# Performance work log

Measured on AMD Instinct MI355X. Metric: run time of the kernel, lower is better.

## Reference

```python
import jax, jax.numpy as jnp
import numpy as np

LEAK = 0.01  # torch LeakyReLU default negative_slope

def lrelu(x):
    return jnp.where(x >= 0, x, LEAK * x)

def edge_conv(x, src, dst, ea, W1, b1, W2, b2):
    # message: cat(x_i=target, x_j=source, edge_attr) -> Linear -> LeakyReLU -> Linear
    m = jnp.concatenate([x[dst], x[src], ea], axis=1)          # [E, 2F+Fe]
    h = lrelu(m @ W1 + b1) @ W2 + b2                            # [E, H]
    n = x.shape[0]
    agg = jnp.full((n, h.shape[1]), jnp.inf, h.dtype).at[dst].min(h)  # scatter-min at target
    return jnp.where(jnp.isfinite(agg), agg, jnp.zeros_like(agg))     # empty nodes -> 0


def setup_inputs() -> dict:
    key = jax.random.key(0)
    ks = jax.random.split(key, 20)
    B, N, E = 4, 20000, 640000
    NF, AD, EF, H = 2, 1, 1, 8
    inp = {
        "node_features": jax.random.randint(ks[0], (B, N, NF), 0, 10, dtype=jnp.int32),
        "actions": jax.random.normal(ks[1], (B, N), dtype=jnp.float32),
        "edge_index": jax.random.randint(ks[2], (B, 2, E), 0, N, dtype=jnp.int64),
        "edge_features": jax.random.normal(ks[3], (B, E, EF), dtype=jnp.float32),
    }
    d0 = NF + AD  # 3
    def lin(k, fin, fout):
        s = 1.0 / np.sqrt(fin)
        k1, k2 = jax.random.split(k)
        return (jax.random.uniform(k1, (fin, fout), jnp.float32, -s, s),
                jax.random.uniform(k2, (fout,), jnp.float32, -s, s))
    inp["c1_W1"], inp["c1_b1"] = lin(ks[4], 2 * d0 + EF, H)
    inp["c1_W2"], inp["c1_b2"] = lin(ks[5], H, H)
    inp["c2_W1"], inp["c2_b1"] = lin(ks[6], 2 * H + 1, H)
    inp["c2_W2"], inp["c2_b2"] = lin(ks[7], H, H)
    inp["c3_W1"], inp["c3_b1"] = lin(ks[8], 2 * H + 1, H)
    inp["c3_W2"], inp["c3_b2"] = lin(ks[9], H, H)
    inp["lin_W"], inp["lin_b"] = lin(ks[10], d0 + H, 1)
    return inp


def reference(node_features, actions, edge_index, edge_features,
              c1_W1, c1_b1, c1_W2, c1_b2,
              c2_W1, c2_b1, c2_W2, c2_b2,
              c3_W1, c3_b1, c3_W2, c3_b2,
              lin_W, lin_b):
    # x = int(node_features) concat actions  -> float
    x0 = jnp.concatenate([node_features.astype(jnp.int32).astype(jnp.float32),
                          actions[..., None]], axis=-1)  # [B,N,3]

    def per_graph(x0g, eig, eag):
        src, dst = eig[0], eig[1]  # flow source_to_target: x_j=src, x_i=dst
        h = lrelu(edge_conv(x0g, src, dst, eag, c1_W1, c1_b1, c1_W2, c1_b2))
        h = lrelu(edge_conv(h, src, dst, eag, c2_W1, c2_b1, c2_W2, c2_b2))
        h = lrelu(edge_conv(h, src, dst, eag, c3_W1, c3_b1, c3_W2, c3_b2))
        xc = jnp.concatenate([x0g, h], axis=1)  # [N, 3+8]
        return jnp.sum(xc, axis=0)              # sum-pool over nodes

    pooled = jax.vmap(per_graph)(x0, edge_index, edge_features)  # [B, 11]
    return pooled @ lin_W + lin_b  # [B, 1]
```

## Files before the change

kernel.cpp:

```cpp
#include <hip/hip_runtime.h>
#include <hip/hip_cooperative_groups.h>

namespace cg = cooperative_groups;

#define LEAK 0.01f
#define BS 128
#define PCHUNK 4096
#define PT 512
#define CT 512
#define MAXNB 256
#define CPGMAX 256

__device__ __forceinline__ float lrelu(float v) {
    return v >= 0.f ? v : LEAK * v;
}

__device__ __forceinline__ unsigned int fmin_encode(float x) {
    unsigned int u = __float_as_uint(x);
    return (u & 0x80000000u) ? ~u : (u | 0x80000000u);
}
__device__ __forceinline__ float fmin_decode(unsigned int k) {
    unsigned int u = (k & 0x80000000u) ? (k ^ 0x80000000u) : ~k;
    return __uint_as_float(u);
}

__device__ __forceinline__ unsigned int bf16_rne(float f) {
    unsigned int u = __float_as_uint(f);
    return (u + 0x7FFFu + ((u >> 16) & 1u)) >> 16;
}

__device__ __forceinline__ void block_add(float c, float* dst) {
    __shared__ float wsum[8];
#pragma unroll
    for (int off = 32; off > 0; off >>= 1) c += __shfl_down(c, off, 64);
    int lane = threadIdx.x & 63;
    int wave = threadIdx.x >> 6;
    if (lane == 0) wsum[wave] = c;
    __syncthreads();
    if (threadIdx.x == 0) {
        float s = 0.f;
        int nw = blockDim.x >> 6;
        for (int w = 0; w < nw; ++w) s += wsum[w];
        atomicAdd(dst, s);
    }
}


__device__ void init_slice_body(
    const int* __restrict__ nf, const float* __restrict__ act,
    const float* __restrict__ W1, const float* __restrict__ b1,
    const float* __restrict__ lw, const float* __restrict__ lb,
    float* __restrict__ a1, unsigned short* __restrict__ a2,
    float* __restrict__ out, int N, int b, int n0, int n1) {
    int t = threadIdx.x;
    float c = 0.f;
    for (int n = n0 + t; n < n1; n += PT) {
        size_t i = (size_t)b * N + n;
        float x0 = (float)nf[i * 2 + 0];
        float x1 = (float)nf[i * 2 + 1];
        float x2 = act[i];
        float v1[8], v2[8];
#pragma unroll
        for (int j = 0; j < 8; ++j) {
            v1[j] = b1[j] + x0 * W1[0 * 8 + j] + x1 * W1[1 * 8 + j] + x2 * W1[2 * 8 + j];
            v2[j] =         x0 * W1[3 * 8 + j] + x1 * W1[4 * 8 + j] + x2 * W1[5 * 8 + j];
        }
        float4* o1 = (float4*)(a1 + i * 8);
        o1[0] = make_float4(v1[0], v1[1], v1[2], v1[3]);
        o1[1] = make_float4(v1[4], v1[5], v1[6], v1[7]);
        unsigned int w[4];
#pragma unroll
        for (int q = 0; q < 4; ++q)
            w[q] = bf16_rne(v2[2 * q]) | (bf16_rne(v2[2 * q + 1]) << 16);
        *(int4*)(a2 + i * 8) = make_int4(w[0], w[1], w[2], w[3]);
        c += x0 * lw[0] + x1 * lw[1] + x2 * lw[2];
        if (n == 0) c += lb[0];
    }
    block_add(c, &out[b]);
}

__device__ void part_body(
    const int* __restrict__ ei, const float* __restrict__ ea,
    int2* __restrict__ pairs, int* __restrict__ ofs,
    int E, int NB, int CPG, int b, int c,
    int* __restrict__ lc, int* __restrict__ lofs, int* __restrict__ ts) {
    int t = threadIdx.x;
    for (int i = t; i < NB; i += PT) lc[i] = 0;
    __syncthreads();

    int e0 = c * PCHUNK;
    int end = min(e0 + PCHUNK, E);
    const int* srow = ei + (size_t)b * 2 * E;
    const int* drow = srow + E;

    int pk[PCHUNK / PT];
#pragma unroll
    for (int j = 0; j < PCHUNK / PT; ++j) {
        int e = e0 + j * PT + t;
        int p = -1;
        if (e < end) {
            int d = drow[e];
            int bin = d >> 7;
            int r = atomicAdd(&lc[bin], 1);
            p = bin | ((d & 127) << 10) | (r << 17);
        }
        pk[j] = p;
    }
    __syncthreads();

    int v = (t < NB) ? lc[t] : 0;
    ts[t] = v;
    __syncthreads();
    int incl = v;
    for (int off = 1; off < PT; off <<= 1) {
        int add = (t >= off) ? ts[t - off] : 0;
        __syncthreads();
        incl += add;
        ts[t] = incl;
        __syncthreads();
    }
    if (t < NB) lofs[t] = incl - v;
    if (t == PT - 1) lofs[NB] = incl;
    __syncthreads();

    for (int i = t; i <= NB; i += PT) {
        int w = lofs[i];
        ofs[((size_t)b * (NB + 1) + i) * CPG + c] = w;
        if (i < NB) lc[i] = w;
    }
    __syncthreads();

    size_t pbase = (size_t)b * E + e0;
#pragma unroll
    for (int j = 0; j < PCHUNK / PT; ++j) {
        int e = e0 + j * PT + t;
        if (e < end) {
            int p = pk[j];
            int bin = p & 1023;
            int dl = (p >> 10) & 127;
            int r = p >> 17;
            int pos = lc[bin] + r;
            pairs[pbase + pos] =
                make_int2(srow[e] | (dl << 16), __float_as_int(ea[(size_t)b * E + e]));
        }
    }
}

__device__ __forceinline__ void conv_edge_compute(
    const float* we, const float* bb, const float* __restrict__ W2,
    int2 p, int4 raw, const float* __restrict__ a1s,
    unsigned int* __restrict__ acc) {
    int dl = (p.x >> 16) & 127;
    float eav = __int_as_float(p.y);
    unsigned int wq[4] = {(unsigned int)raw.x, (unsigned int)raw.y,
                          (unsigned int)raw.z, (unsigned int)raw.w};
    float a2v[8];
#pragma unroll
    for (int q = 0; q < 4; ++q) {
        a2v[2 * q]     = __uint_as_float(wq[q] << 16);
        a2v[2 * q + 1] = __uint_as_float(wq[q] & 0xFFFF0000u);
    }
    float h1[8];
#pragma unroll
    for (int j = 0; j < 8; ++j) {
        h1[j] = a1s[dl * 9 + j] + a2v[j];
        h1[j] = fmaf(eav, we[j], h1[j]);
        h1[j] = lrelu(h1[j]);
    }
    float h2[8];
#pragma unroll
    for (int j = 0; j < 8; ++j) h2[j] = bb[j];
#pragma unroll
    for (int kk = 0; kk < 8; ++kk) {
        float hk = h1[kk];
#pragma unroll
        for (int j = 0; j < 8; ++j) h2[j] = fmaf(hk, W2[kk * 8 + j], h2[j]);
    }
#pragma unroll
    for (int j = 0; j < 8; ++j)
        atomicMin(&acc[dl * 9 + j], fmin_encode(h2[j]));
}

__device__ void conv_edges_runs(
    const unsigned short* __restrict__ a2g, const float* we, const float* bb,
    const float* __restrict__ W2, const int2* __restrict__ pairsg,
    const int* __restrict__ ofb, int CPG,
    const float* __restrict__ a1s, unsigned int* __restrict__ acc,
    int* __restrict__ rs, int* __restrict__ re) {
    int t = threadIdx.x;
    for (int c = t; c < CPG; c += CT) {
        rs[c] = ofb[c];
        re[c] = ofb[CPG + c];
    }
    __syncthreads();
    int sw = t >> 5, sub = t & 31;
    const int nsw = CT >> 5;
    for (int c = sw; c < CPG; c += nsw) {
        int cb = c * PCHUNK;
        int k1 = cb + re[c];
        for (int k = cb + rs[c] + sub; k < k1; k += 32) {
            int2 p = pairsg[k];
            int4 v = *(const int4*)(a2g + (size_t)(p.x & 0xFFFF) * 8);
            conv_edge_compute(we, bb, W2, p, v, a1s, acc);
        }
    }
}

__device__ void conv_mid_body(
    const float* __restrict__ a1, const unsigned short* __restrict__ a2,
    const float* __restrict__ w1e, const float* __restrict__ W2,
    const float* __restrict__ b2,
    const float* __restrict__ nW1, const float* __restrict__ nb1,
    const int* __restrict__ ofs, const int2* __restrict__ pairs,
    float* __restrict__ na1, unsigned short* __restrict__ na2,
    int N, int NB, int CPG, int E, int b, int bin,
    float* __restrict__ a1s, unsigned int* __restrict__ acc,
    int* __restrict__ rs, int* __restrict__ re) {
    int n0 = bin << 7;
    int nCnt = min(BS, N - n0);
    int t = threadIdx.x;
    size_t node0 = (size_t)b * N + n0;

    for (int i = t; i < nCnt * 8; i += CT)
        a1s[(i >> 3) * 9 + (i & 7)] = a1[node0 * 8 + i];
    for (int i = t; i < BS * 9; i += CT) acc[i] = 0xFFFFFFFFu;
    float we[8], bb[8];
#pragma unroll
    for (int j = 0; j < 8; ++j) { we[j] = w1e[j]; bb[j] = b2[j]; }
    __syncthreads();

    conv_edges_runs(a2 + (size_t)b * N * 8, we, bb, W2,
                    pairs + (size_t)b * E,
                    ofs + ((size_t)b * (NB + 1) + bin) * CPG,
                    CPG, a1s, acc, rs, re);
    __syncthreads();

    for (int i = t; i < nCnt * 8; i += CT) {
        float v = fmin_decode(acc[(i >> 3) * 9 + (i & 7)]);
        unsigned int u = __float_as_uint(v);
        if ((u & 0x7F800000u) == 0x7F800000u) v = 0.f;
        a1s[(i >> 3) * 9 + (i & 7)] = lrelu(v);
    }
    __syncthreads();

    for (int nh = t; nh < nCnt * 2; nh += CT) {
        int node = nh >> 1, half = nh & 1;
        float h[8];
#pragma unroll
        for (int j = 0; j < 8; ++j) h[j] = a1s[node * 9 + j];
        float v[8];
#pragma unroll
        for (int j = 0; j < 8; ++j) v[j] = half ? 0.f : nb1[j];
        const float* Wbase = nW1 + (half ? 64 : 0);
#pragma unroll
        for (int k = 0; k < 8; ++k) {
            float hk = h[k];
#pragma unroll
            for (int j = 0; j < 8; ++j) v[j] = fmaf(hk, Wbase[k * 8 + j], v[j]);
        }
        if (half) {
            unsigned int w[4];
#pragma unroll
            for (int q = 0; q < 4; ++q)
                w[q] = bf16_rne(v[2 * q]) | (bf16_rne(v[2 * q + 1]) << 16);
            *(int4*)(na2 + (node0 + node) * 8) = make_int4(w[0], w[1], w[2], w[3]);
        } else {
            float4* o = (float4*)(na1 + (node0 + node) * 8);
            o[0] = make_float4(v[0], v[1], v[2], v[3]);
            o[1] = make_float4(v[4], v[5], v[6], v[7]);
        }
    }
    __syncthreads();
}

__device__ void conv_final_body(
    const float* __restrict__ a1, const unsigned short* __restrict__ a2,
    const float* __restrict__ w1e, const float* __restrict__ W2,
    const float* __restrict__ b2, const float* __restrict__ lw,
    const int* __restrict__ ofs, const int2* __restrict__ pairs,
    float* __restrict__ out, int N, int NB, int CPG, int E, int b, int bin,
    float* __restrict__ a1s, unsigned int* __restrict__ acc,
    int* __restrict__ rs, int* __restrict__ re) {
    int n0 = bin << 7;
    int nCnt = min(BS, N - n0);
    int t = threadIdx.x;
    size_t node0 = (size_t)b * N + n0;

    for (int i = t; i < nCnt * 8; i += CT)
        a1s[(i >> 3) * 9 + (i & 7)] = a1[node0 * 8 + i];
    for (int i = t; i < BS * 9; i += CT) acc[i] = 0xFFFFFFFFu;
    float we[8], bb[8];
#pragma unroll
    for (int j = 0; j < 8; ++j) { we[j] = w1e[j]; bb[j] = b2[j]; }
    __syncthreads();

    conv_edges_runs(a2 + (size_t)b * N * 8, we, bb, W2,
                    pairs + (size_t)b * E,
                    ofs + ((size_t)b * (NB + 1) + bin) * CPG,
                    CPG, a1s, acc, rs, re);
    __syncthreads();

    float c = 0.f;
    if (t < nCnt) {
#pragma unroll
        for (int j = 0; j < 8; ++j) {
            float v = fmin_decode(acc[t * 9 + j]);
            unsigned int u = __float_as_uint(v);
            if ((u & 0x7F800000u) == 0x7F800000u) v = 0.f;
            c = fmaf(lrelu(v), lw[3 + j], c);
        }
    }
    __syncthreads();
    block_add(c, &out[b]);
}


struct MegaParams {
    const int* ei; const float* ea;
    int2* pairs; int* ofs;
    const int* nf; const float* act;
    const float* W11; const float* b11; const float* W21; const float* b21;
    const float* W12; const float* b12; const float* W22; const float* b22;
    const float* W13; const float* b13; const float* W23; const float* b23;
    const float* lw; const float* lb;
    float* a1A; unsigned short* a2A; float* a1B; unsigned short* a2B;
    float* out;
    int E, N, NB, CPG, nodesPerBlock;
};

__global__ __launch_bounds__(512, 8) void mega_kernel(MegaParams P) {
    cg::grid_group grid = cg::this_grid();
    __shared__ int lc[MAXNB];
    __shared__ int lofs[MAXNB + 1];
    __shared__ int ts[PT];
    __shared__ float a1s[BS * 9];
    __shared__ unsigned int acc[BS * 9];
    __shared__ int rs[CPGMAX];
    __shared__ int re[CPGMAX];
    int b = blockIdx.y, bx = blockIdx.x;

    if (bx < P.CPG)
        part_body(P.ei, P.ea, P.pairs, P.ofs, P.E, P.NB, P.CPG, b, bx, lc, lofs, ts);
    {
        int n0 = bx * P.nodesPerBlock;
        int n1 = min(n0 + P.nodesPerBlock, P.N);
        if (n0 < P.N)
            init_slice_body(P.nf, P.act, P.W11, P.b11, P.lw, P.lb,
                            P.a1A, P.a2A, P.out, P.N, b, n0, n1);
        else
            block_add(0.f, P.out + b);
    }
    __threadfence();
    grid.sync();
    if (bx < P.NB)
        conv_mid_body(P.a1A, P.a2A, P.W11 + 6 * 8, P.W21, P.b21, P.W12, P.b12,
                      P.ofs, P.pairs, P.a1B, P.a2B, P.N, P.NB, P.CPG, P.E,
                      b, bx, a1s, acc, rs, re);
    __threadfence();
    grid.sync();
    if (bx < P.NB)
        conv_mid_body(P.a1B, P.a2B, P.W12 + 16 * 8, P.W22, P.b22, P.W13, P.b13,
                      P.ofs, P.pairs, P.a1A, P.a2A, P.N, P.NB, P.CPG, P.E,
                      b, bx, a1s, acc, rs, re);
    __threadfence();
    grid.sync();
    if (bx < P.NB)
        conv_final_body(P.a1A, P.a2A, P.W13 + 16 * 8, P.W23, P.b23, P.lw,
                        P.ofs, P.pairs, P.out, P.N, P.NB, P.CPG, P.E,
                        b, bx, a1s, acc, rs, re);
}


__global__ __launch_bounds__(PT) void part_init_kernel(
    const int* __restrict__ ei, const float* __restrict__ ea,
    int2* __restrict__ pairs, int* __restrict__ ofs,
    const int* __restrict__ nf, const float* __restrict__ act,
    const float* __restrict__ W1, const float* __restrict__ b1,
    const float* __restrict__ lw, const float* __restrict__ lb,
    float* __restrict__ a1, unsigned short* __restrict__ a2,
    float* __restrict__ out, int E, int N, int NB, int CPG) {
    __shared__ int lc[MAXNB];
    __shared__ int lofs[MAXNB + 1];
    __shared__ int ts[PT];
    int b = blockIdx.y;
    if (blockIdx.x >= CPG) {
        int n0 = (blockIdx.x - CPG) * PT;
        init_slice_body(nf, act, W1, b1, lw, lb, a1, a2, out, N, b,
                        n0, min(n0 + PT, N));
        return;
    }
    part_body(ei, ea, pairs, ofs, E, NB, CPG, b, blockIdx.x, lc, lofs, ts);
}

__global__ __launch_bounds__(CT) void conv_mid_kernel(
    const float* __restrict__ a1, const unsigned short* __restrict__ a2,
    const float* __restrict__ w1e, const float* __restrict__ W2,
    const float* __restrict__ b2,
    const float* __restrict__ nW1, const float* __restrict__ nb1,
    const int* __restrict__ ofs, const int2* __restrict__ pairs,
    float* __restrict__ na1, unsigned short* __restrict__ na2,
    int N, int NB, int CPG, int E) {
    __shared__ float a1s[BS * 9];
    __shared__ unsigned int acc[BS * 9];
    __shared__ int rs[CPGMAX];
    __shared__ int re[CPGMAX];
    conv_mid_body(a1, a2, w1e, W2, b2, nW1, nb1, ofs, pairs, na1, na2,
                  N, NB, CPG, E, blockIdx.y, blockIdx.x, a1s, acc, rs, re);
}

__global__ __launch_bounds__(CT) void conv_final_kernel(
    const float* __restrict__ a1, const unsigned short* __restrict__ a2,
    const float* __restrict__ w1e, const float* __restrict__ W2,
    const float* __restrict__ b2, const float* __restrict__ lw,
    const int* __restrict__ ofs, const int2* __restrict__ pairs,
    float* __restrict__ out, int N, int NB, int CPG, int E) {
    __shared__ float a1s[BS * 9];
    __shared__ unsigned int acc[BS * 9];
    __shared__ int rs[CPGMAX];
    __shared__ int re[CPGMAX];
    conv_final_body(a1, a2, w1e, W2, b2, lw, ofs, pairs, out,
                    N, NB, CPG, E, blockIdx.y, blockIdx.x, a1s, acc, rs, re);
}


__global__ __launch_bounds__(256) void node_init_kernel(
    const int* __restrict__ nf, const float* __restrict__ act,
    float* __restrict__ x0, int BN) {
    int tid = blockIdx.x * blockDim.x + threadIdx.x;
    if (tid >= BN) return;
    x0[tid * 3 + 0] = (float)nf[tid * 2 + 0];
    x0[tid * 3 + 1] = (float)nf[tid * 2 + 1];
    x0[tid * 3 + 2] = act[tid];
}

template <int D>
__global__ __launch_bounds__(256) void edge_conv_kernel(
    const float* __restrict__ x, const int* __restrict__ ei,
    const float* __restrict__ ea,
    const float* __restrict__ W1, const float* __restrict__ b1,
    const float* __restrict__ W2, const float* __restrict__ b2,
    unsigned int* __restrict__ agg, int E, int N, int B) {
    int tid = blockIdx.x * blockDim.x + threadIdx.x;
    if (tid >= B * E) return;
    int b = tid / E;
    int e = tid - b * E;
    const int* eb = ei + (size_t)b * 2 * E;
    int s = eb[e];
    int d = eb[E + e];
    const float* xi = x + ((size_t)b * N + d) * D;
    const float* xj = x + ((size_t)b * N + s) * D;
    constexpr int M = 2 * D + 1;
    float m[M];
#pragma unroll
    for (int k = 0; k < D; ++k) { m[k] = xi[k]; m[D + k] = xj[k]; }
    m[2 * D] = ea[(size_t)b * E + e];
    float h1[8];
#pragma unroll
    for (int j = 0; j < 8; ++j) h1[j] = b1[j];
#pragma unroll
    for (int k = 0; k < M; ++k) {
        float mk = m[k];
#pragma unroll
        for (int j = 0; j < 8; ++j) h1[j] = fmaf(mk, W1[k * 8 + j], h1[j]);
    }
#pragma unroll
    for (int j = 0; j < 8; ++j) h1[j] = lrelu(h1[j]);
    float h2[8];
#pragma unroll
    for (int j = 0; j < 8; ++j) h2[j] = b2[j];
#pragma unroll
    for (int k = 0; k < 8; ++k) {
        float hk = h1[k];
#pragma unroll
        for (int j = 0; j < 8; ++j) h2[j] = fmaf(hk, W2[k * 8 + j], h2[j]);
    }
    unsigned int* ag = agg + ((size_t)b * N + d) * 8;
#pragma unroll
    for (int j = 0; j < 8; ++j) atomicMin(&ag[j], fmin_encode(h2[j]));
}

__global__ __launch_bounds__(256) void finalize_kernel(
    unsigned int* __restrict__ agg, int total) {
    int tid = blockIdx.x * blockDim.x + threadIdx.x;
    if (tid >= total) return;
    float v = fmin_decode(agg[tid]);
    unsigned int u = __float_as_uint(v);
    if ((u & 0x7F800000u) == 0x7F800000u) v = 0.f;
    ((float*)agg)[tid] = lrelu(v);
}

__global__ __launch_bounds__(256) void pool_kernel(
    const float* __restrict__ x0, const float* __restrict__ h,
    const float* __restrict__ lw, const float* __restrict__ lb,
    float* __restrict__ out, int N) {
    int b = blockIdx.y;
    int n = blockIdx.x * blockDim.x + threadIdx.x;
    float c = 0.f;
    if (n < N) {
        const float* x = x0 + ((size_t)b * N + n) * 3;
        const float* hh = h + ((size_t)b * N + n) * 8;
        c = x[0] * lw[0] + x[1] * lw[1] + x[2] * lw[2];
#pragma unroll
        for (int k = 0; k < 8; ++k) c = fmaf(hh[k], lw[3 + k], c);
        if (n == 0) c += lb[0];
    }
    block_add(c, &out[b]);
}


static inline size_t align256(size_t x) { return (x + 255) & ~(size_t)255; }

extern "C" void kernel_launch(void* const* d_in, const int* in_sizes, int n_in,
                              void* d_out, int out_size, void* d_ws, size_t ws_size,
                              hipStream_t stream) {
    const int B = 4;
    const int N = in_sizes[1] / B;
    const int E = in_sizes[2] / (2 * B);

    const int*   nf  = (const int*)d_in[0];
    const float* act = (const float*)d_in[1];
    const int*   ei  = (const int*)d_in[2];
    const float* ea  = (const float*)d_in[3];
    const float* c1_W1 = (const float*)d_in[4];
    const float* c1_b1 = (const float*)d_in[5];
    const float* c1_W2 = (const float*)d_in[6];
    const float* c1_b2 = (const float*)d_in[7];
    const float* c2_W1 = (const float*)d_in[8];
    const float* c2_b1 = (const float*)d_in[9];
    const float* c2_W2 = (const float*)d_in[10];
    const float* c2_b2 = (const float*)d_in[11];
    const float* c3_W1 = (const float*)d_in[12];
    const float* c3_b1 = (const float*)d_in[13];
    const float* c3_W2 = (const float*)d_in[14];
    const float* c3_b2 = (const float*)d_in[15];
    const float* lw    = (const float*)d_in[16];
    const float* lb    = (const float*)d_in[17];
    float* out = (float*)d_out;

    const int BN = B * N;
    const int BE = B * E;
    const int NB = (N + BS - 1) / BS;
    const int CPG = (E + PCHUNK - 1) / PCHUNK;

    char* ws = (char*)d_ws;
    size_t off = 0;
    float* a1A = (float*)(ws + off);           off += align256((size_t)BN * 8 * 4);
    float* a1B = (float*)(ws + off);           off += align256((size_t)BN * 8 * 4);
    unsigned short* a2A = (unsigned short*)(ws + off); off += align256((size_t)BN * 8 * 2);
    unsigned short* a2B = (unsigned short*)(ws + off); off += align256((size_t)BN * 8 * 2);
    int* ofs    = (int*)(ws + off);    off += align256((size_t)B * (NB + 1) * CPG * 4);
    int2* pairs = (int2*)(ws + off);   off += align256((size_t)BE * 8);
    float* x0   = (float*)(ws + off);  off += align256((size_t)BN * 3 * 4);
    const bool useFast = (off <= ws_size) && (NB <= MAXNB) && (CPG <= CPGMAX) &&
                         (N <= 32768);

    hipMemsetAsync(out, 0, (size_t)B * sizeof(float), stream);

    if (useFast) {
        const int gx = (CPG > NB) ? CPG : NB;
        const int nodesPerBlock = (N + gx - 1) / gx;

        int dev = 0;
        hipGetDevice(&dev);
        int numCU = 0;
        hipDeviceGetAttribute(&numCU, hipDeviceAttributeMultiprocessorCount, dev);
        int occ = 0;
        hipOccupancyMaxActiveBlocksPerMultiprocessor(&occ, mega_kernel, 512, 0);
        const bool canCoop = (occ > 0) && ((size_t)occ * (size_t)numCU >=
                                           (size_t)gx * (size_t)B);

        if (canCoop) {
            MegaParams P;
            P.ei = ei; P.ea = ea; P.pairs = pairs; P.ofs = ofs;
            P.nf = nf; P.act = act;
            P.W11 = c1_W1; P.b11 = c1_b1; P.W21 = c1_W2; P.b21 = c1_b2;
            P.W12 = c2_W1; P.b12 = c2_b1; P.W22 = c2_W2; P.b22 = c2_b2;
            P.W13 = c3_W1; P.b13 = c3_b1; P.W23 = c3_W2; P.b23 = c3_b2;
            P.lw = lw; P.lb = lb;
            P.a1A = a1A; P.a2A = a2A; P.a1B = a1B; P.a2B = a2B;
            P.out = out;
            P.E = E; P.N = N; P.NB = NB; P.CPG = CPG;
            P.nodesPerBlock = nodesPerBlock;
            void* args[] = {&P};
            hipLaunchCooperativeKernel((void*)mega_kernel, dim3(gx, B),
                                       dim3(512), args, 0, stream);
        } else {
            const int initBlocks = (N + PT - 1) / PT;
            dim3 pgrid(CPG + initBlocks, B);
            dim3 cgrid(NB, B);
            part_init_kernel<<<pgrid, PT, 0, stream>>>(
                ei, ea, pairs, ofs, nf, act, c1_W1, c1_b1, lw, lb,
                a1A, a2A, out, E, N, NB, CPG);
            conv_mid_kernel<<<cgrid, CT, 0, stream>>>(
                a1A, a2A, c1_W1 + 6 * 8, c1_W2, c1_b2, c2_W1, c2_b1,
                ofs, pairs, a1B, a2B, N, NB, CPG, E);
            conv_mid_kernel<<<cgrid, CT, 0, stream>>>(
                a1B, a2B, c2_W1 + 16 * 8, c2_W2, c2_b2, c3_W1, c3_b1,
                ofs, pairs, a1A, a2A, N, NB, CPG, E);
            conv_final_kernel<<<cgrid, CT, 0, stream>>>(
                a1A, a2A, c3_W1 + 16 * 8, c3_W2, c3_b2, lw,
                ofs, pairs, out, N, NB, CPG, E);
        }
    } else {
        const int egrid = (BE + 255) / 256;
        const int aggTotal = BN * 8;
        const int agrid = (aggTotal + 255) / 256;
        const size_t aggBytes = (size_t)aggTotal * 4;
        unsigned int* uA = (unsigned int*)a1A;
        unsigned int* uB = (unsigned int*)a1B;

        node_init_kernel<<<(BN + 255) / 256, 256, 0, stream>>>(nf, act, x0, BN);

        hipMemsetAsync(uA, 0xFF, aggBytes, stream);
        edge_conv_kernel<3><<<egrid, 256, 0, stream>>>(
            x0, ei, ea, c1_W1, c1_b1, c1_W2, c1_b2, uA, E, N, B);
        finalize_kernel<<<agrid, 256, 0, stream>>>(uA, aggTotal);

        hipMemsetAsync(uB, 0xFF, aggBytes, stream);
        edge_conv_kernel<8><<<egrid, 256, 0, stream>>>(
            (const float*)uA, ei, ea, c2_W1, c2_b1, c2_W2, c2_b2, uB, E, N, B);
        finalize_kernel<<<agrid, 256, 0, stream>>>(uB, aggTotal);

        hipMemsetAsync(uA, 0xFF, aggBytes, stream);
        edge_conv_kernel<8><<<egrid, 256, 0, stream>>>(
            (const float*)uB, ei, ea, c3_W1, c3_b1, c3_W2, c3_b2, uA, E, N, B);
        finalize_kernel<<<agrid, 256, 0, stream>>>(uA, aggTotal);

        dim3 plgrid((N + 255) / 256, B);
        pool_kernel<<<plgrid, 256, 0, stream>>>(x0, (const float*)uA, lw, lb, out, N);
    }
}
```

Before: 208.4 us.

## Add per-bin counting sort of edges by destination to cut shared atomics

Adds a sort phase that counting-sorts each bin's edges by local destination node into a contiguous segment array, using global per-bin counts to compute segment offsets. The conv phases then give each thread a contiguous run of edges, keep a register-resident running min, and issue shared atomicMin only when the destination changes, instead of eight atomics per edge. Shared memory is merged into a union, which frees LDS for occupancy, and the launch bound drops to 6 blocks per CU. The cost is an extra grid sync plus a read and write of all edge pairs, and uneven per-thread runs could cause load imbalance.

```diff
diff --git a/kernel.cpp b/kernel.cpp
--- a/kernel.cpp
+++ b/kernel.cpp
@@ -44,6 +44,11 @@
         atomicAdd(dst, s);
     }
 }
+
+struct SmemPart { int lc[MAXNB]; int lofs[MAXNB + 1]; int ts[PT]; };
+struct SmemSort { int rs[CPGMAX]; int re[CPGMAX]; int hist[BS]; int cursor[BS]; int red[PT / 64]; };
+struct SmemConv { float a1s[BS * 9]; unsigned int acc[BS * 9]; };
+union SmemU { SmemPart p; SmemSort s; SmemConv c; };
 
 
 __device__ void init_slice_body(
@@ -81,11 +86,10 @@
 
 __device__ void part_body(
     const int* __restrict__ ei, const float* __restrict__ ea,
-    int2* __restrict__ pairs, int* __restrict__ ofs,
-    int E, int NB, int CPG, int b, int c,
-    int* __restrict__ lc, int* __restrict__ lofs, int* __restrict__ ts) {
+    int2* __restrict__ pairs, int* __restrict__ ofs, int* __restrict__ bcnt,
+    int E, int NB, int CPG, int b, int c, SmemPart* sm) {
     int t = threadIdx.x;
-    for (int i = t; i < NB; i += PT) lc[i] = 0;
+    for (int i = t; i < NB; i += PT) sm->lc[i] = 0;
     __syncthreads();
 
     int e0 = c * PCHUNK;
@@ -101,32 +105,33 @@
         if (e < end) {
             int d = drow[e];
             int bin = d >> 7;
-            int r = atomicAdd(&lc[bin], 1);
+            int r = atomicAdd(&sm->lc[bin], 1);
             p = bin | ((d & 127) << 10) | (r << 17);
         }
         pk[j] = p;
     }
     __syncthreads();
 
-    int v = (t < NB) ? lc[t] : 0;
-    ts[t] = v;
+    int v = (t < NB) ? sm->lc[t] : 0;
+    if (t < NB && v) atomicAdd(&bcnt[b * NB + t], v);
+    sm->ts[t] = v;
     __syncthreads();
     int incl = v;
     for (int off = 1; off < PT; off <<= 1) {
-        int add = (t >= off) ? ts[t - off] : 0;
+        int add = (t >= off) ? sm->ts[t - off] : 0;
         __syncthreads();
         incl += add;
-        ts[t] = incl;
+        sm->ts[t] = incl;
         __syncthreads();
     }
-    if (t < NB) lofs[t] = incl - v;
-    if (t == PT - 1) lofs[NB] = incl;
+    if (t < NB) sm->lofs[t] = incl - v;
+    if (t == PT - 1) sm->lofs[NB] = incl;
     __syncthreads();
 
     for (int i = t; i <= NB; i += PT) {
-        int w = lofs[i];
+        int w = sm->lofs[i];
         ofs[((size_t)b * (NB + 1) + i) * CPG + c] = w;
-        if (i < NB) lc[i] = w;
+        if (i < NB) sm->lc[i] = w;
     }
     __syncthreads();
 
@@ -139,70 +144,135 @@
             int bin = p & 1023;
             int dl = (p >> 10) & 127;
             int r = p >> 17;
-            int pos = lc[bin] + r;
+            int pos = sm->lc[bin] + r;
             pairs[pbase + pos] =
                 make_int2(srow[e] | (dl << 16), __float_as_int(ea[(size_t)b * E + e]));
         }
     }
 }
 
-__device__ __forceinline__ void conv_edge_compute(
-    const float* we, const float* bb, const float* __restrict__ W2,
-    int2 p, int4 raw, const float* __restrict__ a1s,
-    unsigned int* __restrict__ acc) {
-    int dl = (p.x >> 16) & 127;
-    float eav = __int_as_float(p.y);
-    unsigned int wq[4] = {(unsigned int)raw.x, (unsigned int)raw.y,
-                          (unsigned int)raw.z, (unsigned int)raw.w};
-    float a2v[8];
-#pragma unroll
-    for (int q = 0; q < 4; ++q) {
-        a2v[2 * q]     = __uint_as_float(wq[q] << 16);
-        a2v[2 * q + 1] = __uint_as_float(wq[q] & 0xFFFF0000u);
-    }
-    float h1[8];
-#pragma unroll
-    for (int j = 0; j < 8; ++j) {
-        h1[j] = a1s[dl * 9 + j] + a2v[j];
-        h1[j] = fmaf(eav, we[j], h1[j]);
-        h1[j] = lrelu(h1[j]);
-    }
-    float h2[8];
-#pragma unroll
-    for (int j = 0; j < 8; ++j) h2[j] = bb[j];
-#pragma unroll
-    for (int kk = 0; kk < 8; ++kk) {
-        float hk = h1[kk];
-#pragma unroll
-        for (int j = 0; j < 8; ++j) h2[j] = fmaf(hk, W2[kk * 8 + j], h2[j]);
-    }
-#pragma unroll
-    for (int j = 0; j < 8; ++j)
-        atomicMin(&acc[dl * 9 + j], fmin_encode(h2[j]));
-}
-
-__device__ void conv_edges_runs(
-    const unsigned short* __restrict__ a2g, const float* we, const float* bb,
-    const float* __restrict__ W2, const int2* __restrict__ pairsg,
-    const int* __restrict__ ofb, int CPG,
-    const float* __restrict__ a1s, unsigned int* __restrict__ acc,
-    int* __restrict__ rs, int* __restrict__ re) {
+__device__ void sort_body(
+    const int* __restrict__ ofs_bbin,
+    const int* __restrict__ bcnt_b,
+    const int2* __restrict__ pairsg,
+    int2* __restrict__ spairsg,
+    int* __restrict__ segofs_b,
+    int NB, int CPG, int bin, SmemSort* sm) {
     int t = threadIdx.x;
-    for (int c = t; c < CPG; c += CT) {
-        rs[c] = ofb[c];
-        re[c] = ofb[CPG + c];
-    }
-    __syncthreads();
+    for (int c = t; c < CPG; c += PT) {
+        sm->rs[c] = ofs_bbin[c];
+        sm->re[c] = ofs_bbin[CPG + c];
+    }
+    for (int i = t; i < BS; i += PT) sm->hist[i] = 0;
+
+    int part = 0;
+    for (int i = t; i < bin; i += PT) part += bcnt_b[i];
+#pragma unroll
+    for (int off = 32; off > 0; off >>= 1) part += __shfl_down(part, off, 64);
+    if ((t & 63) == 0) sm->red[t >> 6] = part;
+    __syncthreads();
+    if (t == 0) {
+        int s = 0;
+        for (int w = 0; w < PT / 64; ++w) s += sm->red[w];
+        sm->red[0] = s;
+    }
+    __syncthreads();
+    int seg0 = sm->red[0];
+    int cnt = bcnt_b[bin];
+    if (t == 0) {
+        segofs_b[bin] = seg0;
+        if (bin == NB - 1) segofs_b[NB] = seg0 + cnt;
+    }
+
     int sw = t >> 5, sub = t & 31;
-    const int nsw = CT >> 5;
+    const int nsw = PT >> 5;
     for (int c = sw; c < CPG; c += nsw) {
         int cb = c * PCHUNK;
-        int k1 = cb + re[c];
-        for (int k = cb + rs[c] + sub; k < k1; k += 32) {
+        int k1 = cb + sm->re[c];
+        for (int k = cb + sm->rs[c] + sub; k < k1; k += 32)
+            atomicAdd(&sm->hist[(pairsg[k].x >> 16) & 127], 1);
+    }
+    __syncthreads();
+
+    if (t < BS) sm->cursor[t] = sm->hist[t];
+    __syncthreads();
+    for (int off = 1; off < BS; off <<= 1) {
+        int add = 0;
+        if (t < BS && t >= off) add = sm->cursor[t - off];
+        __syncthreads();
+        if (t < BS) sm->cursor[t] += add;
+        __syncthreads();
+    }
+    if (t < BS) sm->cursor[t] -= sm->hist[t];
+    __syncthreads();
+
+    for (int c = sw; c < CPG; c += nsw) {
+        int cb = c * PCHUNK;
+        int k1 = cb + sm->re[c];
+        for (int k = cb + sm->rs[c] + sub; k < k1; k += 32) {
             int2 p = pairsg[k];
-            int4 v = *(const int4*)(a2g + (size_t)(p.x & 0xFFFF) * 8);
-            conv_edge_compute(we, bb, W2, p, v, a1s, acc);
-        }
+            int pos = atomicAdd(&sm->cursor[(p.x >> 16) & 127], 1);
+            spairsg[seg0 + pos] = p;
+        }
+    }
+}
+
+__device__ void conv_core(
+    const unsigned short* __restrict__ a2g, const float* we, const float* bb,
+    const float* __restrict__ W2, const int2* __restrict__ spairsg,
+    int seg0, int seg1, const float* __restrict__ a1s,
+    unsigned int* __restrict__ acc) {
+    int t = threadIdx.x;
+    int len = seg1 - seg0;
+    int per = (len + CT - 1) / CT;
+    int k0 = seg0 + t * per;
+    int k1 = min(k0 + per, seg1);
+    int curdl = -1;
+    float m[8];
+    for (int k = k0; k < k1; ++k) {
+        int2 p = spairsg[k];
+        int dl = (p.x >> 16) & 127;
+        if (dl != curdl) {
+            if (curdl >= 0) {
+#pragma unroll
+                for (int j = 0; j < 8; ++j)
+                    atomicMin(&acc[curdl * 9 + j], fmin_encode(m[j]));
+            }
+            curdl = dl;
+#pragma unroll
+            for (int j = 0; j < 8; ++j) m[j] = __builtin_inff();
+        }
+        float eav = __int_as_float(p.y);
+        int4 raw = *(const int4*)(a2g + (size_t)(p.x & 0xFFFF) * 8);
+        unsigned int wq[4] = {(unsigned int)raw.x, (unsigned int)raw.y,
+                              (unsigned int)raw.z, (unsigned int)raw.w};
+        float h1[8];
+#pragma unroll
+        for (int q = 0; q < 4; ++q) {
+            h1[2 * q]     = a1s[dl * 9 + 2 * q]     + __uint_as_float(wq[q] << 16);
+            h1[2 * q + 1] = a1s[dl * 9 + 2 * q + 1] + __uint_as_float(wq[q] & 0xFFFF0000u);
+        }
+#pragma unroll
+        for (int j = 0; j < 8; ++j) {
+            h1[j] = fmaf(eav, we[j], h1[j]);
+            h1[j] = lrelu(h1[j]);
+        }
+        float h2[8];
+#pragma unroll
+        for (int j = 0; j < 8; ++j) h2[j] = bb[j];
+#pragma unroll
+        for (int kk = 0; kk < 8; ++kk) {
+            float hk = h1[kk];
+#pragma unroll
+            for (int j = 0; j < 8; ++j) h2[j] = fmaf(hk, W2[kk * 8 + j], h2[j]);
+        }
+#pragma unroll
+        for (int j = 0; j < 8; ++j) m[j] = fminf(m[j], h2[j]);
+    }
+    if (curdl >= 0) {
+#pragma unroll
+        for (int j = 0; j < 8; ++j)
+            atomicMin(&acc[curdl * 9 + j], fmin_encode(m[j]));
     }
 }
 
@@ -211,35 +281,33 @@
     const float* __restrict__ w1e, const float* __restrict__ W2,
     const float* __restrict__ b2,
     const float* __restrict__ nW1, const float* __restrict__ nb1,
-    const int* __restrict__ ofs, const int2* __restrict__ pairs,
+    const int* __restrict__ segofs, const int2* __restrict__ spairs,
     float* __restrict__ na1, unsigned short* __restrict__ na2,
-    int N, int NB, int CPG, int E, int b, int bin,
-    float* __restrict__ a1s, unsigned int* __restrict__ acc,
-    int* __restrict__ rs, int* __restrict__ re) {
+    int N, int NB, int E, int b, int bin, SmemConv* sm) {
     int n0 = bin << 7;
     int nCnt = min(BS, N - n0);
     int t = threadIdx.x;
     size_t node0 = (size_t)b * N + n0;
 
     for (int i = t; i < nCnt * 8; i += CT)
-        a1s[(i >> 3) * 9 + (i & 7)] = a1[node0 * 8 + i];
-    for (int i = t; i < BS * 9; i += CT) acc[i] = 0xFFFFFFFFu;
+        sm->a1s[(i >> 3) * 9 + (i & 7)] = a1[node0 * 8 + i];
+    for (int i = t; i < BS * 9; i += CT) sm->acc[i] = 0xFFFFFFFFu;
     float we[8], bb[8];
 #pragma unroll
     for (int j = 0; j < 8; ++j) { we[j] = w1e[j]; bb[j] = b2[j]; }
-    __syncthreads();
-
-    conv_edges_runs(a2 + (size_t)b * N * 8, we, bb, W2,
-                    pairs + (size_t)b * E,
-                    ofs + ((size_t)b * (NB + 1) + bin) * CPG,
-                    CPG, a1s, acc, rs, re);
+    const int* so = segofs + (size_t)b * (NB + 1);
+    int seg0 = so[bin], seg1 = so[bin + 1];
+    __syncthreads();
+
+    conv_core(a2 + (size_t)b * N * 8, we, bb, W2, spairs + (size_t)b * E,
+              seg0, seg1, sm->a1s, sm->acc);
     __syncthreads();
 
     for (int i = t; i < nCnt * 8; i += CT) {
-        float v = fmin_decode(acc[(i >> 3) * 9 + (i & 7)]);
+        float v = fmin_decode(sm->acc[(i >> 3) * 9 + (i & 7)]);
         unsigned int u = __float_as_uint(v);
         if ((u & 0x7F800000u) == 0x7F800000u) v = 0.f;
-        a1s[(i >> 3) * 9 + (i & 7)] = lrelu(v);
+        sm->a1s[(i >> 3) * 9 + (i & 7)] = lrelu(v);
     }
     __syncthreads();
 
@@ -247,7 +315,7 @@
         int node = nh >> 1, half = nh & 1;
         float h[8];
 #pragma unroll
-        for (int j = 0; j < 8; ++j) h[j] = a1s[node * 9 + j];
+        for (int j = 0; j < 8; ++j) h[j] = sm->a1s[node * 9 + j];
         float v[8];
 #pragma unroll
         for (int j = 0; j < 8; ++j) v[j] = half ? 0.f : nb1[j];
@@ -277,34 +345,33 @@
     const float* __restrict__ a1, const unsigned short* __restrict__ a2,
     const float* __restrict__ w1e, const float* __restrict__ W2,
     const float* __restrict__ b2, const float* __restrict__ lw,
-    const int* __restrict__ ofs, const int2* __restrict__ pairs,
-    float* __restrict__ out, int N, int NB, int CPG, int E, int b, int bin,
-    float* __restrict__ a1s, unsigned int* __restrict__ acc,
-    int* __restrict__ rs, int* __restrict__ re) {
+    const int* __restrict__ segofs, const int2* __restrict__ spairs,
+    float* __restrict__ out, int N, int NB, int E, int b, int bin,
+    SmemConv* sm) {
     int n0 = bin << 7;
     int nCnt = min(BS, N - n0);
     int t = threadIdx.x;
     size_t node0 = (size_t)b * N + n0;
 
     for (int i = t; i < nCnt * 8; i += CT)
-        a1s[(i >> 3) * 9 + (i & 7)] = a1[node0 * 8 + i];
-    for (int i = t; i < BS * 9; i += CT) acc[i] = 0xFFFFFFFFu;
+        sm->a1s[(i >> 3) * 9 + (i & 7)] = a1[node0 * 8 + i];
+    for (int i = t; i < BS * 9; i += CT) sm->acc[i] = 0xFFFFFFFFu;
     float we[8], bb[8];
 #pragma unroll
     for (int j = 0; j < 8; ++j) { we[j] = w1e[j]; bb[j] = b2[j]; }
-    __syncthreads();
-
-    conv_edges_runs(a2 + (size_t)b * N * 8, we, bb, W2,
-                    pairs + (size_t)b * E,
-                    ofs + ((size_t)b * (NB + 1) + bin) * CPG,
-                    CPG, a1s, acc, rs, re);
+    const int* so = segofs + (size_t)b * (NB + 1);
+    int seg0 = so[bin], seg1 = so[bin + 1];
+    __syncthreads();
+
+    conv_core(a2 + (size_t)b * N * 8, we, bb, W2, spairs + (size_t)b * E,
+              seg0, seg1, sm->a1s, sm->acc);
     __syncthreads();
 
     float c = 0.f;
     if (t < nCnt) {
 #pragma unroll
         for (int j = 0; j < 8; ++j) {
-            float v = fmin_decode(acc[t * 9 + j]);
+            float v = fmin_decode(sm->acc[t * 9 + j]);
             unsigned int u = __float_as_uint(v);
             if ((u & 0x7F800000u) == 0x7F800000u) v = 0.f;
             c = fmaf(lrelu(v), lw[3 + j], c);
@@ -317,7 +384,7 @@
 
 struct MegaParams {
     const int* ei; const float* ea;
-    int2* pairs; int* ofs;
+    int2* pairs; int2* spairs; int* ofs; int* bcnt; int* segofs;
     const int* nf; const float* act;
     const float* W11; const float* b11; const float* W21; const float* b21;
     const float* W12; const float* b12; const float* W22; const float* b22;
@@ -328,19 +395,13 @@
     int E, N, NB, CPG, nodesPerBlock;
 };
 
-__global__ __launch_bounds__(512, 8) void mega_kernel(MegaParams P) {
+__global__ __launch_bounds__(512, 6) void mega_kernel(MegaParams P) {
     cg::grid_group grid = cg::this_grid();
-    __shared__ int lc[MAXNB];
-    __shared__ int lofs[MAXNB + 1];
-    __shared__ int ts[PT];
-    __shared__ float a1s[BS * 9];
-    __shared__ unsigned int acc[BS * 9];
-    __shared__ int rs[CPGMAX];
-    __shared__ int re[CPGMAX];
+    __shared__ SmemU sm;
     int b = blockIdx.y, bx = blockIdx.x;
 
     if (bx < P.CPG)
-        part_body(P.ei, P.ea, P.pairs, P.ofs, P.E, P.NB, P.CPG, b, bx, lc, lofs, ts);
+        part_body(P.ei, P.ea, P.pairs, P.ofs, P.bcnt, P.E, P.NB, P.CPG, b, bx, &sm.p);
     {
         int n0 = bx * P.nodesPerBlock;
         int n1 = min(n0 + P.nodesPerBlock, P.N);
@@ -353,35 +414,39 @@
     __threadfence();
     grid.sync();
     if (bx < P.NB)
+        sort_body(P.ofs + ((size_t)b * (P.NB + 1) + bx) * P.CPG,
+                  P.bcnt + (size_t)b * P.NB,
+                  P.pairs + (size_t)b * P.E, P.spairs + (size_t)b * P.E,
+                  P.segofs + (size_t)b * (P.NB + 1), P.NB, P.CPG, bx, &sm.s);
+    __threadfence();
+    grid.sync();
+    if (bx < P.NB)
         conv_mid_body(P.a1A, P.a2A, P.W11 + 6 * 8, P.W21, P.b21, P.W12, P.b12,
-                      P.ofs, P.pairs, P.a1B, P.a2B, P.N, P.NB, P.CPG, P.E,
-                      b, bx, a1s, acc, rs, re);
+                      P.segofs, P.spairs, P.a1B, P.a2B, P.N, P.NB, P.E,
+                      b, bx, &sm.c);
     __threadfence();
     grid.sync();
     if (bx < P.NB)
         conv_mid_body(P.a1B, P.a2B, P.W12 + 16 * 8, P.W22, P.b22, P.W13, P.b13,
-                      P.ofs, P.pairs, P.a1A, P.a2A, P.N, P.NB, P.CPG, P.E,
-                      b, bx, a1s, acc, rs, re);
+                      P.segofs, P.spairs, P.a1A, P.a2A, P.N, P.NB, P.E,
+                      b, bx, &sm.c);
     __threadfence();
     grid.sync();
     if (bx < P.NB)
         conv_final_body(P.a1A, P.a2A, P.W13 + 16 * 8, P.W23, P.b23, P.lw,
-                        P.ofs, P.pairs, P.out, P.N, P.NB, P.CPG, P.E,
-                        b, bx, a1s, acc, rs, re);
+                        P.segofs, P.spairs, P.out, P.N, P.NB, P.E, b, bx, &sm.c);
 }
 
 
 __global__ __launch_bounds__(PT) void part_init_kernel(
     const int* __restrict__ ei, const float* __restrict__ ea,
-    int2* __restrict__ pairs, int* __restrict__ ofs,
+    int2* __restrict__ pairs, int* __restrict__ ofs, int* __restrict__ bcnt,
     const int* __restrict__ nf, const float* __restrict__ act,
     const float* __restrict__ W1, const float* __restrict__ b1,
     const float* __restrict__ lw, const float* __restrict__ lb,
     float* __restrict__ a1, unsigned short* __restrict__ a2,
     float* __restrict__ out, int E, int N, int NB, int CPG) {
-    __shared__ int lc[MAXNB];
-    __shared__ int lofs[MAXNB + 1];
-    __shared__ int ts[PT];
+    __shared__ SmemPart sm;
     int b = blockIdx.y;
     if (blockIdx.x >= CPG) {
         int n0 = (blockIdx.x - CPG) * PT;
@@ -389,7 +454,18 @@
                         n0, min(n0 + PT, N));
         return;
     }
-    part_body(ei, ea, pairs, ofs, E, NB, CPG, b, blockIdx.x, lc, lofs, ts);
+    part_body(ei, ea, pairs, ofs, bcnt, E, NB, CPG, b, blockIdx.x, &sm);
+}
+
+__global__ __launch_bounds__(PT) void sort_kernel(
+    const int* __restrict__ ofs, const int* __restrict__ bcnt,
+    const int2* __restrict__ pairs, int2* __restrict__ spairs,
+    int* __restrict__ segofs, int NB, int CPG, int E) {
+    __shared__ SmemSort sm;
+    int b = blockIdx.y, bin = blockIdx.x;
+    sort_body(ofs + ((size_t)b * (NB + 1) + bin) * CPG, bcnt + (size_t)b * NB,
+              pairs + (size_t)b * E, spairs + (size_t)b * E,
+              segofs + (size_t)b * (NB + 1), NB, CPG, bin, &sm);
 }
 
 __global__ __launch_bounds__(CT) void conv_mid_kernel(
@@ -397,29 +473,23 @@
     const float* __restrict__ w1e, const float* __restrict__ W2,
     const float* __restrict__ b2,
     const float* __restrict__ nW1, const float* __restrict__ nb1,
-    const int* __restrict__ ofs, const int2* __restrict__ pairs,
+    const int* __restrict__ segofs, const int2* __restrict__ spairs,
     float* __restrict__ na1, unsigned short* __restrict__ na2,
-    int N, int NB, int CPG, int E) {
-    __shared__ float a1s[BS * 9];
-    __shared__ unsigned int acc[BS * 9];
-    __shared__ int rs[CPGMAX];
-    __shared__ int re[CPGMAX];
-    conv_mid_body(a1, a2, w1e, W2, b2, nW1, nb1, ofs, pairs, na1, na2,
-                  N, NB, CPG, E, blockIdx.y, blockIdx.x, a1s, acc, rs, re);
+    int N, int NB, int E) {
+    __shared__ SmemConv sm;
+    conv_mid_body(a1, a2, w1e, W2, b2, nW1, nb1, segofs, spairs, na1, na2,
+                  N, NB, E, blockIdx.y, blockIdx.x, &sm);
 }
 
 __global__ __launch_bounds__(CT) void conv_final_kernel(
     const float* __restrict__ a1, const unsigned short* __restrict__ a2,
     const float* __restrict__ w1e, const float* __restrict__ W2,
     const float* __restrict__ b2, const float* __restrict__ lw,
-    const int* __restrict__ ofs, const int2* __restrict__ pairs,
-    float* __restrict__ out, int N, int NB, int CPG, int E) {
-    __shared__ float a1s[BS * 9];
-    __shared__ unsigned int acc[BS * 9];
-    __shared__ int rs[CPGMAX];
-    __shared__ int re[CPGMAX];
-    conv_final_body(a1, a2, w1e, W2, b2, lw, ofs, pairs, out,
-                    N, NB, CPG, E, blockIdx.y, blockIdx.x, a1s, acc, rs, re);
+    const int* __restrict__ segofs, const int2* __restrict__ spairs,
+    float* __restrict__ out, int N, int NB, int E) {
+    __shared__ SmemConv sm;
+    conv_final_body(a1, a2, w1e, W2, b2, lw, segofs, spairs, out,
+                    N, NB, E, blockIdx.y, blockIdx.x, &sm);
 }
 
 
@@ -549,7 +619,10 @@
     unsigned short* a2A = (unsigned short*)(ws + off); off += align256((size_t)BN * 8 * 2);
     unsigned short* a2B = (unsigned short*)(ws + off); off += align256((size_t)BN * 8 * 2);
     int* ofs    = (int*)(ws + off);    off += align256((size_t)B * (NB + 1) * CPG * 4);
+    int* bcnt   = (int*)(ws + off);    off += align256((size_t)B * NB * 4);
+    int* segofs = (int*)(ws + off);    off += align256((size_t)B * (NB + 1) * 4);
     int2* pairs = (int2*)(ws + off);   off += align256((size_t)BE * 8);
+    int2* spairs = (int2*)(ws + off);  off += align256((size_t)BE * 8);
     float* x0   = (float*)(ws + off);  off += align256((size_t)BN * 3 * 4);
     const bool useFast = (off <= ws_size) && (NB <= MAXNB) && (CPG <= CPGMAX) &&
                          (N <= 32768);
@@ -557,6 +630,7 @@
     hipMemsetAsync(out, 0, (size_t)B * sizeof(float), stream);
 
     if (useFast) {
+        hipMemsetAsync(bcnt, 0, (size_t)B * NB * 4, stream);
         const int gx = (CPG > NB) ? CPG : NB;
         const int nodesPerBlock = (N + gx - 1) / gx;
 
@@ -571,7 +645,8 @@
 
         if (canCoop) {
             MegaParams P;
-            P.ei = ei; P.ea = ea; P.pairs = pairs; P.ofs = ofs;
+            P.ei = ei; P.ea = ea; P.pairs = pairs; P.spairs = spairs;
+            P.ofs = ofs; P.bcnt = bcnt; P.segofs = segofs;
             P.nf = nf; P.act = act;
             P.W11 = c1_W1; P.b11 = c1_b1; P.W21 = c1_W2; P.b21 = c1_b2;
             P.W12 = c2_W1; P.b12 = c2_b1; P.W22 = c2_W2; P.b22 = c2_b2;
@@ -589,17 +664,19 @@
             dim3 pgrid(CPG + initBlocks, B);
             dim3 cgrid(NB, B);
             part_init_kernel<<<pgrid, PT, 0, stream>>>(
-                ei, ea, pairs, ofs, nf, act, c1_W1, c1_b1, lw, lb,
+                ei, ea, pairs, ofs, bcnt, nf, act, c1_W1, c1_b1, lw, lb,
                 a1A, a2A, out, E, N, NB, CPG);
+            sort_kernel<<<cgrid, PT, 0, stream>>>(ofs, bcnt, pairs, spairs,
+                                                  segofs, NB, CPG, E);
             conv_mid_kernel<<<cgrid, CT, 0, stream>>>(
                 a1A, a2A, c1_W1 + 6 * 8, c1_W2, c1_b2, c2_W1, c2_b1,
-                ofs, pairs, a1B, a2B, N, NB, CPG, E);
+                segofs, spairs, a1B, a2B, N, NB, E);
             conv_mid_kernel<<<cgrid, CT, 0, stream>>>(
                 a1B, a2B, c2_W1 + 16 * 8, c2_W2, c2_b2, c3_W1, c3_b1,
-                ofs, pairs, a1A, a2A, N, NB, CPG, E);
+                segofs, spairs, a1A, a2A, N, NB, E);
             conv_final_kernel<<<cgrid, CT, 0, stream>>>(
                 a1A, a2A, c3_W1 + 16 * 8, c3_W2, c3_b2, lw,
-                ofs, pairs, out, N, NB, CPG, E);
+                segofs, spairs, out, N, NB, E);
         }
     } else {
         const int egrid = (BE + 255) / 256;
```

After: 256.4 us. 1.23x slower.
